# Kernel optimization log

Measured on AMD Instinct MI355X. Metric: run time of the kernel, lower is better.

The kernel has to match this reference:

```python
import jax, jax.numpy as jnp
import numpy as np

D_MODEL = 512
NUM_HEADS = 8
DEPTH = D_MODEL // NUM_HEADS


def setup_inputs() -> dict:
    key = jax.random.key(0)
    ks = jax.random.split(key, 11)
    B, S = 2, 4096
    scale = 1.0 / np.sqrt(D_MODEL)
    inp = {
        "q": jax.random.normal(ks[0], (B, S, D_MODEL), jnp.float32),
        "k": jax.random.normal(ks[1], (B, S, D_MODEL), jnp.float32),
        "v": jax.random.normal(ks[2], (B, S, D_MODEL), jnp.float32),
        "wq_w": jax.random.normal(ks[3], (D_MODEL, D_MODEL), jnp.float32) * scale,
        "wq_b": jnp.zeros((D_MODEL,), jnp.float32),
        "wk_w": jax.random.normal(ks[4], (D_MODEL, D_MODEL), jnp.float32) * scale,
        "wk_b": jnp.zeros((D_MODEL,), jnp.float32),
        "wv_w": jax.random.normal(ks[5], (D_MODEL, D_MODEL), jnp.float32) * scale,
        "wv_b": jnp.zeros((D_MODEL,), jnp.float32),
        "wo_w": jax.random.normal(ks[6], (D_MODEL, D_MODEL), jnp.float32) * scale,
        "wo_b": jnp.zeros((D_MODEL,), jnp.float32),
    }
    return inp


def _split_heads(x):
    # [B, S, D] -> [B, H, S, depth]
    B, S, _ = x.shape
    return x.reshape(B, S, NUM_HEADS, DEPTH).transpose(0, 2, 1, 3)


def reference(q, k, v, wq_w, wq_b, wk_w, wk_b, wv_w, wv_b, wo_w, wo_b):
    B, S, _ = q.shape
    qh = _split_heads(q @ wq_w.T + wq_b)  # [B,H,S,d]
    kh = _split_heads(k @ wk_w.T + wk_b)
    vh = _split_heads(v @ wv_w.T + wv_b)
    logits = jnp.einsum('bhqd,bhkd->bhqk', qh, kh) / jnp.sqrt(
        jnp.asarray(DEPTH, jnp.float32))
    attn = jax.nn.softmax(logits, axis=-1)
    out = jnp.einsum('bhqk,bhkd->bhqd', attn, vh)  # [B,H,S,d]
    out = out.transpose(0, 2, 1, 3).reshape(B, S, D_MODEL)
    return out @ wo_w.T + wo_b
```

## Files before the change

kernel.cpp:

```cpp
#include <hip/hip_runtime.h>

typedef __attribute__((ext_vector_type(8))) short short8;
typedef __attribute__((ext_vector_type(4))) float float4v;

#define D_MODEL 512
#define NUM_HEADS 8
#define DEPTH 64
#define SEQ 4096
#define BATCH 2
#define MROWS 8192
#define SCALE_Q 0.18033688011112043f

#define SW(r, c) (((r) * 64) + ((((c) ^ ((r) & 7))) * 8))
#define SW128(n, c) (((n) * 128) + ((((c) ^ ((n) & 15))) * 8))

static __device__ __forceinline__ unsigned short f2bf(float f) {
  unsigned int u = __builtin_bit_cast(unsigned int, f);
  u += 0x7FFFu + ((u >> 16) & 1u);
  return (unsigned short)(u >> 16);
}
static __device__ __forceinline__ unsigned int pk2(float a, float b) {
  return (unsigned int)f2bf(a) | ((unsigned int)f2bf(b) << 16);
}
static __device__ __forceinline__ unsigned int pk2f(float a, float b) {
  unsigned int ua = __builtin_bit_cast(unsigned int, a) + 0x8000u;
  unsigned int ub = __builtin_bit_cast(unsigned int, b) + 0x8000u;
  return __builtin_amdgcn_perm(ub, ua, 0x07060302u);
}

struct CvtArgs {
  const float4v* src[7];
  uint2* dst[7];
  int n4[7];
};
__global__ __launch_bounds__(256) void cvt_all(CvtArgs a) {
  const int ti = blockIdx.y;
  const float4v* __restrict__ s = a.src[ti];
  uint2* __restrict__ d = a.dst[ti];
  const int n = a.n4[ti];
  for (int i = blockIdx.x * 256 + threadIdx.x; i < n; i += gridDim.x * 256) {
    float4v f = s[i];
    d[i] = make_uint2(pk2(f[0], f[1]), pk2(f[2], f[3]));
  }
}

struct QkvArgs {
  const unsigned short* X[3];
  const unsigned short* W[3];
  const float* bias[3];
  unsigned short* out[3];
};
__global__ __launch_bounds__(256) void gemm128_qkv(QkvArgs a) {
  __shared__ unsigned short smem[2 * 128 * 64];
  unsigned short* As = smem;
  unsigned short* Bs = smem + 128 * 64;
  const int z = blockIdx.z;
  const unsigned short* __restrict__ X = a.X[z];
  const unsigned short* __restrict__ W = a.W[z];
  const float* __restrict__ bias = a.bias[z];
  unsigned short* __restrict__ out = a.out[z];
  const int t = threadIdx.x;
  const int w = t >> 6, l = t & 63, lq = l >> 4, lm = l & 15;
  const int mq = (w & 1) * 64, nq = (w >> 1) * 64;
  const int mBase = blockIdx.x * 128, nBase = blockIdx.y * 128;
  float4v acc[4][4] = {};
  for (int kc = 0; kc < D_MODEL; kc += 64) {
    __syncthreads();
#pragma unroll
    for (int p = 0; p < 4; ++p) {
      int i = p * 256 + t, r = i >> 3, c = i & 7;
      *(short8*)&As[SW(r, c)] = *(const short8*)&X[(size_t)(mBase + r) * D_MODEL + kc + c * 8];
      *(short8*)&Bs[SW(r, c)] = *(const short8*)&W[(size_t)(nBase + r) * D_MODEL + kc + c * 8];
    }
    __syncthreads();
#pragma unroll
    for (int kk = 0; kk < 2; ++kk) {
      short8 av[4];
#pragma unroll
      for (int fm = 0; fm < 4; ++fm)
        av[fm] = *(const short8*)&As[SW(mq + fm * 16 + lm, kk * 4 + lq)];
#pragma unroll
      for (int fn = 0; fn < 4; ++fn) {
        short8 bv = *(const short8*)&Bs[SW(nq + fn * 16 + lm, kk * 4 + lq)];
#pragma unroll
        for (int fm = 0; fm < 4; ++fm)
          acc[fm][fn] = __builtin_amdgcn_mfma_f32_16x16x32_bf16(av[fm], bv, acc[fm][fn], 0, 0, 0);
      }
    }
  }
  if (z == 2) {
    __syncthreads();
    unsigned short* T = smem;
#pragma unroll
    for (int fn = 0; fn < 4; ++fn) {
      int n = nq + fn * 16 + lm;
      float bv = bias[nBase + n];
#pragma unroll
      for (int fm = 0; fm < 4; ++fm) {
        int m0 = mq + fm * 16 + lq * 4;
        uint2 u;
        u.x = pk2(acc[fm][fn][0] + bv, acc[fm][fn][1] + bv);
        u.y = pk2(acc[fm][fn][2] + bv, acc[fm][fn][3] + bv);
        *(uint2*)&T[SW128(n, m0 >> 3) + (lq & 1) * 4] = u;
      }
    }
    __syncthreads();
    const int bb = mBase >> 12, s0 = mBase & 4095;
#pragma unroll
    for (int p = 0; p < 8; ++p) {
      int i = p * 256 + t, n = i >> 4, cm = i & 15;
      int gn = nBase + n, h = gn >> 6, d = gn & 63;
      *(short8*)&out[(((size_t)(bb * NUM_HEADS + h) * DEPTH + d) << 12) + s0 + cm * 8] =
          *(const short8*)&T[SW128(n, cm)];
    }
  } else {
    const float scale = (z == 0) ? SCALE_Q : 1.0f;
#pragma unroll
    for (int fn = 0; fn < 4; ++fn) {
      int gn = nBase + nq + fn * 16 + lm;
      float bv = bias[gn];
      int h = gn >> 6, d = gn & 63;
#pragma unroll
      for (int fm = 0; fm < 4; ++fm) {
#pragma unroll
        for (int r = 0; r < 4; ++r) {
          int gm = mBase + mq + fm * 16 + lq * 4 + r;
          int bb = gm >> 12, s = gm & 4095;
          out[(((size_t)(bb * NUM_HEADS + h) * SEQ + s) << 6) + d] =
              f2bf((acc[fm][fn][r] + bv) * scale);
        }
      }
    }
  }
}

__global__ __launch_bounds__(256) void gemm128_out(
    const unsigned short* __restrict__ X, const unsigned short* __restrict__ W,
    const float* __restrict__ bias, float* __restrict__ out) {
  __shared__ unsigned short smem[2 * 128 * 64];
  unsigned short* As = smem;
  unsigned short* Bs = smem + 128 * 64;
  const int t = threadIdx.x;
  const int w = t >> 6, l = t & 63, lq = l >> 4, lm = l & 15;
  const int mq = (w & 1) * 64, nq = (w >> 1) * 64;
  const int mBase = blockIdx.x * 128, nBase = blockIdx.y * 128;
  float4v acc[4][4] = {};
  for (int kc = 0; kc < D_MODEL; kc += 64) {
    __syncthreads();
#pragma unroll
    for (int p = 0; p < 4; ++p) {
      int i = p * 256 + t, r = i >> 3, c = i & 7;
      *(short8*)&As[SW(r, c)] = *(const short8*)&X[(size_t)(mBase + r) * D_MODEL + kc + c * 8];
      *(short8*)&Bs[SW(r, c)] = *(const short8*)&W[(size_t)(nBase + r) * D_MODEL + kc + c * 8];
    }
    __syncthreads();
#pragma unroll
    for (int kk = 0; kk < 2; ++kk) {
      short8 av[4];
#pragma unroll
      for (int fm = 0; fm < 4; ++fm)
        av[fm] = *(const short8*)&As[SW(mq + fm * 16 + lm, kk * 4 + lq)];
#pragma unroll
      for (int fn = 0; fn < 4; ++fn) {
        short8 bv = *(const short8*)&Bs[SW(nq + fn * 16 + lm, kk * 4 + lq)];
#pragma unroll
        for (int fm = 0; fm < 4; ++fm)
          acc[fm][fn] = __builtin_amdgcn_mfma_f32_16x16x32_bf16(av[fm], bv, acc[fm][fn], 0, 0, 0);
      }
    }
  }
#pragma unroll
  for (int fn = 0; fn < 4; ++fn) {
    int gn = nBase + nq + fn * 16 + lm;
    float bv = bias[gn];
#pragma unroll
    for (int fm = 0; fm < 4; ++fm) {
#pragma unroll
      for (int r = 0; r < 4; ++r) {
        int gm = mBase + mq + fm * 16 + lq * 4 + r;
        out[(size_t)gm * D_MODEL + gn] = acc[fm][fn][r] + bv;
      }
    }
  }
}

struct QkvArgsF {
  const void* X[3];
  const void* W[3];
  const float* bias[3];
  unsigned short* out[3];
};
template <int XFP32, int WFP32>
__global__ __launch_bounds__(256) void gemm_qkv(QkvArgsF a) {
  __shared__ unsigned short As[64 * 72];
  __shared__ unsigned short Bs[64 * 72];
  const int z = blockIdx.z;
  const void* __restrict__ Xv = a.X[z];
  const void* __restrict__ Wv = a.W[z];
  const float* __restrict__ bias = a.bias[z];
  unsigned short* __restrict__ outv = a.out[z];
  const int t = threadIdx.x;
  const int w = t >> 6, l = t & 63, lq = l >> 4, lm = l & 15;
  const int mBase = blockIdx.x * 64;
  const int nBase = blockIdx.y * 64;
  float4v acc[4] = {};
  for (int kc = 0; kc < D_MODEL; kc += 64) {
    __syncthreads();
#pragma unroll
    for (int p = 0; p < 2; ++p) {
      int idx = p * 256 + t;
      int r = idx >> 3, c = (idx & 7) * 8;
      if (XFP32) {
        const float* Xf = (const float*)Xv;
        float4v f0 = *(const float4v*)&Xf[(size_t)(mBase + r) * D_MODEL + kc + c];
        float4v f1 = *(const float4v*)&Xf[(size_t)(mBase + r) * D_MODEL + kc + c + 4];
        short8 s;
#pragma unroll
        for (int j = 0; j < 4; ++j) { s[j] = (short)f2bf(f0[j]); s[4 + j] = (short)f2bf(f1[j]); }
        *(short8*)&As[r * 72 + c] = s;
      } else {
        *(short8*)&As[r * 72 + c] =
            *(const short8*)&((const unsigned short*)Xv)[(size_t)(mBase + r) * D_MODEL + kc + c];
      }
      if (WFP32) {
        const float* Wf = (const float*)Wv;
        float4v f0 = *(const float4v*)&Wf[(size_t)(nBase + r) * D_MODEL + kc + c];
        float4v f1 = *(const float4v*)&Wf[(size_t)(nBase + r) * D_MODEL + kc + c + 4];
        short8 s;
#pragma unroll
        for (int j = 0; j < 4; ++j) { s[j] = (short)f2bf(f0[j]); s[4 + j] = (short)f2bf(f1[j]); }
        *(short8*)&Bs[r * 72 + c] = s;
      } else {
        *(short8*)&Bs[r * 72 + c] =
            *(const short8*)&((const unsigned short*)Wv)[(size_t)(nBase + r) * D_MODEL + kc + c];
      }
    }
    __syncthreads();
#pragma unroll
    for (int kk = 0; kk < 64; kk += 32) {
      short8 av = *(const short8*)&As[(w * 16 + lm) * 72 + kk + lq * 8];
#pragma unroll
      for (int f = 0; f < 4; ++f) {
        short8 b = *(const short8*)&Bs[(f * 16 + lm) * 72 + kk + lq * 8];
        acc[f] = __builtin_amdgcn_mfma_f32_16x16x32_bf16(av, b, acc[f], 0, 0, 0);
      }
    }
  }
  if (z == 2) {
    __syncthreads();
    unsigned short* T = As;
#pragma unroll
    for (int f = 0; f < 4; ++f) {
      int dl = f * 16 + lm;
      float bv = bias[nBase + dl];
      uint2 u;
      u.x = pk2(acc[f][0] + bv, acc[f][1] + bv);
      u.y = pk2(acc[f][2] + bv, acc[f][3] + bv);
      int chunk = 2 * w + (lq >> 1);
      *(uint2*)&T[SW(dl, chunk) + (lq & 1) * 4] = u;
    }
    __syncthreads();
    const int bb = mBase >> 12, s0v = mBase & 4095, h = nBase >> 6;
    const size_t vbase = ((size_t)(bb * NUM_HEADS + h)) * DEPTH * SEQ;
#pragma unroll
    for (int p = 0; p < 2; ++p) {
      int idx = p * 256 + t;
      int d = idx >> 3, c = idx & 7;
      *(short8*)&outv[vbase + (size_t)d * SEQ + s0v + c * 8] = *(const short8*)&T[SW(d, c)];
    }
  } else {
    const float scale = (z == 0) ? SCALE_Q : 1.0f;
#pragma unroll
    for (int f = 0; f < 4; ++f) {
      int gn = nBase + f * 16 + lm;
      float bv = bias[gn];
#pragma unroll
      for (int r = 0; r < 4; ++r) {
        int gm = mBase + w * 16 + lq * 4 + r;
        float v = (acc[f][r] + bv) * scale;
        int bb = gm >> 12, s = gm & 4095;
        int h = gn >> 6, d = gn & 63;
        outv[(((size_t)(bb * NUM_HEADS + h) * SEQ + s) << 6) + d] = f2bf(v);
      }
    }
  }
}

__global__ __launch_bounds__(256) void gemm_out_f(
    const unsigned short* __restrict__ Xb, const float* __restrict__ Wf,
    const float* __restrict__ bias, float* __restrict__ out) {
  __shared__ unsigned short As[64 * 72];
  __shared__ unsigned short Bs[64 * 72];
  const int t = threadIdx.x;
  const int w = t >> 6, l = t & 63, lq = l >> 4, lm = l & 15;
  const int mBase = blockIdx.x * 64;
  const int nBase = blockIdx.y * 64;
  float4v acc[4] = {};
  for (int kc = 0; kc < D_MODEL; kc += 64) {
    __syncthreads();
#pragma unroll
    for (int p = 0; p < 2; ++p) {
      int idx = p * 256 + t;
      int r = idx >> 3, c = (idx & 7) * 8;
      *(short8*)&As[r * 72 + c] =
          *(const short8*)&Xb[(size_t)(mBase + r) * D_MODEL + kc + c];
      float4v f0 = *(const float4v*)&Wf[(size_t)(nBase + r) * D_MODEL + kc + c];
      float4v f1 = *(const float4v*)&Wf[(size_t)(nBase + r) * D_MODEL + kc + c + 4];
      short8 s;
#pragma unroll
      for (int j = 0; j < 4; ++j) { s[j] = (short)f2bf(f0[j]); s[4 + j] = (short)f2bf(f1[j]); }
      *(short8*)&Bs[r * 72 + c] = s;
    }
    __syncthreads();
#pragma unroll
    for (int kk = 0; kk < 64; kk += 32) {
      short8 av = *(const short8*)&As[(w * 16 + lm) * 72 + kk + lq * 8];
#pragma unroll
      for (int f = 0; f < 4; ++f) {
        short8 b = *(const short8*)&Bs[(f * 16 + lm) * 72 + kk + lq * 8];
        acc[f] = __builtin_amdgcn_mfma_f32_16x16x32_bf16(av, b, acc[f], 0, 0, 0);
      }
    }
  }
#pragma unroll
  for (int f = 0; f < 4; ++f) {
    int gn = nBase + f * 16 + lm;
    float bv = bias[gn];
#pragma unroll
    for (int r = 0; r < 4; ++r) {
      int gm = mBase + w * 16 + lq * 4 + r;
      out[(size_t)gm * D_MODEL + gn] = acc[f][r] + bv;
    }
  }
}

__global__ __launch_bounds__(256) void attn(
    const unsigned short* __restrict__ Qh,
    const unsigned short* __restrict__ Kh,
    const unsigned short* __restrict__ Vt,
    unsigned short* __restrict__ AO)
{
  __shared__ unsigned short Ksub[2][64 * 64];
  __shared__ unsigned short Vsub[2][64 * 64];
  __shared__ unsigned short Psub[128 * 64];
  const int t = threadIdx.x;
  const int w = t >> 6;
  const int l = t & 63, lq = l >> 4, lm = l & 15;
  const int bh = blockIdx.y;
  const size_t base = (size_t)bh * SEQ * DEPTH;
  const int qbase = blockIdx.x * 128 + w * 32;
  const unsigned short* __restrict__ Kp = Kh + base;
  const unsigned short* __restrict__ Vp = Vt + base;

  short8 qf[2][2];
#pragma unroll
  for (int qb = 0; qb < 2; ++qb)
#pragma unroll
    for (int kk = 0; kk < 2; ++kk)
      qf[qb][kk] = *(const short8*)&Qh[base + (size_t)(qbase + qb * 16 + lm) * DEPTH + kk * 32 + lq * 8];

  short8 ones;
#pragma unroll
  for (int j = 0; j < 8; ++j) ones[j] = (short)0x3F80;

  float4v oacc[2][4] = {};
  float4v sumacc[2] = {};
  short8 kreg[2], vreg[2];

#pragma unroll
  for (int p = 0; p < 2; ++p) {
    int i = p * 256 + t, r = i >> 3, c = i & 7;
    kreg[p] = *(const short8*)&Kp[(size_t)r * DEPTH + c * 8];
    vreg[p] = *(const short8*)&Vp[(size_t)r * SEQ + c * 8];
  }
#pragma unroll
  for (int p = 0; p < 2; ++p) {
    int i = p * 256 + t, r = i >> 3, c = i & 7;
    *(short8*)&Ksub[0][SW(r, c)] = kreg[p];
    *(short8*)&Vsub[0][SW(r, c)] = vreg[p];
  }
  __syncthreads();

  for (int it = 0; it < 64; ++it) {
    const int cur = it & 1;
    if (it < 63) {
      const int s0n = (it + 1) * 64;
#pragma unroll
      for (int p = 0; p < 2; ++p) {
        int i = p * 256 + t, r = i >> 3, c = i & 7;
        kreg[p] = *(const short8*)&Kp[(size_t)(s0n + r) * DEPTH + c * 8];
        vreg[p] = *(const short8*)&Vp[(size_t)r * SEQ + s0n + c * 8];
      }
    }
#pragma unroll
    for (int f = 0; f < 4; ++f) {
      float4v sacc[2] = {};
#pragma unroll
      for (int kk = 0; kk < 2; ++kk) {
        short8 a = *(const short8*)&Ksub[cur][SW(f * 16 + lm, kk * 4 + lq)];
        sacc[0] = __builtin_amdgcn_mfma_f32_16x16x32_bf16(a, qf[0][kk], sacc[0], 0, 0, 0);
        sacc[1] = __builtin_amdgcn_mfma_f32_16x16x32_bf16(a, qf[1][kk], sacc[1], 0, 0, 0);
      }
#pragma unroll
      for (int qb = 0; qb < 2; ++qb) {
        uint2 u;
        u.x = pk2f(__builtin_amdgcn_exp2f(sacc[qb][0]), __builtin_amdgcn_exp2f(sacc[qb][1]));
        u.y = pk2f(__builtin_amdgcn_exp2f(sacc[qb][2]), __builtin_amdgcn_exp2f(sacc[qb][3]));
        *(uint2*)&Psub[SW(w * 32 + qb * 16 + lm, 2 * f + (lq >> 1)) + (lq & 1) * 4] = u;
      }
    }
#pragma unroll
    for (int kk = 0; kk < 2; ++kk) {
      short8 a0 = *(const short8*)&Psub[SW(w * 32 + lm, kk * 4 + lq)];
      short8 a1 = *(const short8*)&Psub[SW(w * 32 + 16 + lm, kk * 4 + lq)];
      sumacc[0] = __builtin_amdgcn_mfma_f32_16x16x32_bf16(a0, ones, sumacc[0], 0, 0, 0);
      sumacc[1] = __builtin_amdgcn_mfma_f32_16x16x32_bf16(a1, ones, sumacc[1], 0, 0, 0);
#pragma unroll
      for (int df = 0; df < 4; ++df) {
        short8 b = *(const short8*)&Vsub[cur][SW(df * 16 + lm, kk * 4 + lq)];
        oacc[0][df] = __builtin_amdgcn_mfma_f32_16x16x32_bf16(a0, b, oacc[0][df], 0, 0, 0);
        oacc[1][df] = __builtin_amdgcn_mfma_f32_16x16x32_bf16(a1, b, oacc[1][df], 0, 0, 0);
      }
    }
    if (it < 63) {
#pragma unroll
      for (int p = 0; p < 2; ++p) {
        int i = p * 256 + t, r = i >> 3, c = i & 7;
        *(short8*)&Ksub[cur ^ 1][SW(r, c)] = kreg[p];
        *(short8*)&Vsub[cur ^ 1][SW(r, c)] = vreg[p];
      }
    }
    __syncthreads();
  }
  const int bb = bh >> 3, h = bh & 7;
#pragma unroll
  for (int qb = 0; qb < 2; ++qb) {
#pragma unroll
    for (int r = 0; r < 4; ++r) {
      float rinv = 1.0f / sumacc[qb][r];
      int s = qbase + qb * 16 + lq * 4 + r;
#pragma unroll
      for (int df = 0; df < 4; ++df) {
        int d = df * 16 + lm;
        AO[((size_t)(bb * SEQ + s)) * D_MODEL + h * DEPTH + d] = f2bf(oacc[qb][df][r] * rinv);
      }
    }
  }
}

extern "C" void kernel_launch(void* const* d_in, const int* in_sizes, int n_in,
                              void* d_out, int out_size, void* d_ws, size_t ws_size,
                              hipStream_t stream) {
  const void* q = d_in[0];
  const void* k = d_in[1];
  const void* v = d_in[2];
  const float* wq = (const float*)d_in[3];
  const float* bq = (const float*)d_in[4];
  const float* wk = (const float*)d_in[5];
  const float* bk = (const float*)d_in[6];
  const float* wv = (const float*)d_in[7];
  const float* bv = (const float*)d_in[8];
  const float* wo = (const float*)d_in[9];
  const float* bo = (const float*)d_in[10];

  const size_t HSD = (size_t)BATCH * NUM_HEADS * SEQ * DEPTH;
  const size_t WSZ = (size_t)D_MODEL * D_MODEL;
  unsigned short* ws = (unsigned short*)d_ws;
  unsigned short* Qh = ws;
  unsigned short* Kh = Qh + HSD;
  unsigned short* Vt = Kh + HSD;
  unsigned short* AO = Vt + HSD;
  unsigned short* Wc[4] = {AO + HSD, AO + HSD + WSZ, AO + HSD + 2 * WSZ, AO + HSD + 3 * WSZ};
  unsigned short* Xc[3] = {Wc[3] + WSZ, Wc[3] + WSZ + HSD, Wc[3] + WSZ + 2 * HSD};
  const int tier = (ws_size >= (7 * HSD + 4 * WSZ) * 2) ? 1
                 : (ws_size >= (4 * HSD + 4 * WSZ) * 2) ? 2 : 3;

  const float* wptr[4] = {wq, wk, wv, wo};
  const void* xin[3] = {q, k, v};

  if (tier < 3) {
    CvtArgs ca = {};
    int ny = 0;
    if (tier == 1) {
      for (int i = 0; i < 3; ++i) {
        ca.src[ny] = (const float4v*)xin[i];
        ca.dst[ny] = (uint2*)Xc[i];
        ca.n4[ny++] = (int)(HSD / 4);
      }
    }
    for (int i = 0; i < 4; ++i) {
      ca.src[ny] = (const float4v*)wptr[i];
      ca.dst[ny] = (uint2*)Wc[i];
      ca.n4[ny++] = (int)(WSZ / 4);
    }
    cvt_all<<<dim3(512, ny), 256, 0, stream>>>(ca);
  }

  if (tier == 1) {
    QkvArgs qa;
    for (int i = 0; i < 3; ++i) { qa.X[i] = Xc[i]; qa.W[i] = Wc[i]; }
    qa.bias[0] = bq; qa.bias[1] = bk; qa.bias[2] = bv;
    qa.out[0] = Qh; qa.out[1] = Kh; qa.out[2] = Vt;
    gemm128_qkv<<<dim3(MROWS / 128, D_MODEL / 128, 3), 256, 0, stream>>>(qa);
  } else {
    QkvArgsF qa;
    for (int i = 0; i < 3; ++i) qa.X[i] = xin[i];
    qa.bias[0] = bq; qa.bias[1] = bk; qa.bias[2] = bv;
    qa.out[0] = Qh; qa.out[1] = Kh; qa.out[2] = Vt;
    dim3 g(MROWS / 64, D_MODEL / 64, 3);
    if (tier == 2) {
      for (int i = 0; i < 3; ++i) qa.W[i] = Wc[i];
      gemm_qkv<1, 0><<<g, 256, 0, stream>>>(qa);
    } else {
      for (int i = 0; i < 3; ++i) qa.W[i] = wptr[i];
      gemm_qkv<1, 1><<<g, 256, 0, stream>>>(qa);
    }
  }

  attn<<<dim3(SEQ / 128, BATCH * NUM_HEADS), 256, 0, stream>>>(Qh, Kh, Vt, AO);

  if (tier < 3)
    gemm128_out<<<dim3(MROWS / 128, D_MODEL / 128), 256, 0, stream>>>(AO, Wc[3], bo, (float*)d_out);
  else
    gemm_out_f<<<dim3(MROWS / 64, D_MODEL / 64), 256, 0, stream>>>(AO, wo, bo, (float*)d_out);
}
```

Measured before the change: 243.8 us.

## Fuse fp32-to-bf16 conversion into GEMM loads and drop separate convert pass

Removes the standalone cvt_all kernel and the tiered workspace paths. The 128x128 QKV GEMM and a new 128x64 output GEMM now read fp32 inputs and weights directly and convert them to bf16 while filling shared memory. This avoids writing and re-reading bf16 copies of the activations and saves one launch, at the cost of reading twice as many bytes per tile load plus conversion ALU work inside the GEMMs. The attention loop is also manually unrolled by two so the double-buffer index is a compile-time constant.

```diff
diff --git a/kernel.cpp b/kernel.cpp
--- a/kernel.cpp
+++ b/kernel.cpp
@@ -27,36 +27,31 @@
   unsigned int ub = __builtin_bit_cast(unsigned int, b) + 0x8000u;
   return __builtin_amdgcn_perm(ub, ua, 0x07060302u);
 }
-
-struct CvtArgs {
-  const float4v* src[7];
-  uint2* dst[7];
-  int n4[7];
-};
-__global__ __launch_bounds__(256) void cvt_all(CvtArgs a) {
-  const int ti = blockIdx.y;
-  const float4v* __restrict__ s = a.src[ti];
-  uint2* __restrict__ d = a.dst[ti];
-  const int n = a.n4[ti];
-  for (int i = blockIdx.x * 256 + threadIdx.x; i < n; i += gridDim.x * 256) {
-    float4v f = s[i];
-    d[i] = make_uint2(pk2(f[0], f[1]), pk2(f[2], f[3]));
-  }
-}
-
-struct QkvArgs {
-  const unsigned short* X[3];
-  const unsigned short* W[3];
+static __device__ __forceinline__ short8 cvt8(const float* p) {
+  float4v f0 = *(const float4v*)p;
+  float4v f1 = *(const float4v*)(p + 4);
+  short8 s;
+#pragma unroll
+  for (int j = 0; j < 4; ++j) {
+    s[j] = (short)f2bf(f0[j]);
+    s[4 + j] = (short)f2bf(f1[j]);
+  }
+  return s;
+}
+
+struct QkvA {
+  const float* X[3];
+  const float* W[3];
   const float* bias[3];
   unsigned short* out[3];
 };
-__global__ __launch_bounds__(256) void gemm128_qkv(QkvArgs a) {
+__global__ __launch_bounds__(256) void gemm128_qkv(QkvA a) {
   __shared__ unsigned short smem[2 * 128 * 64];
   unsigned short* As = smem;
   unsigned short* Bs = smem + 128 * 64;
   const int z = blockIdx.z;
-  const unsigned short* __restrict__ X = a.X[z];
-  const unsigned short* __restrict__ W = a.W[z];
+  const float* __restrict__ X = a.X[z];
+  const float* __restrict__ W = a.W[z];
   const float* __restrict__ bias = a.bias[z];
   unsigned short* __restrict__ out = a.out[z];
   const int t = threadIdx.x;
@@ -69,8 +64,8 @@
 #pragma unroll
     for (int p = 0; p < 4; ++p) {
       int i = p * 256 + t, r = i >> 3, c = i & 7;
-      *(short8*)&As[SW(r, c)] = *(const short8*)&X[(size_t)(mBase + r) * D_MODEL + kc + c * 8];
-      *(short8*)&Bs[SW(r, c)] = *(const short8*)&W[(size_t)(nBase + r) * D_MODEL + kc + c * 8];
+      *(short8*)&As[SW(r, c)] = cvt8(&X[(size_t)(mBase + r) * D_MODEL + kc + c * 8]);
+      *(short8*)&Bs[SW(r, c)] = cvt8(&W[(size_t)(nBase + r) * D_MODEL + kc + c * 8]);
     }
     __syncthreads();
 #pragma unroll
@@ -134,202 +129,57 @@
   }
 }
 
-__global__ __launch_bounds__(256) void gemm128_out(
-    const unsigned short* __restrict__ X, const unsigned short* __restrict__ W,
-    const float* __restrict__ bias, float* __restrict__ out) {
-  __shared__ unsigned short smem[2 * 128 * 64];
-  unsigned short* As = smem;
-  unsigned short* Bs = smem + 128 * 64;
+__global__ __launch_bounds__(256) void gemm_out_128x64(
+    const unsigned short* __restrict__ X,
+    const float* __restrict__ W,
+    const float* __restrict__ bias,
+    float* __restrict__ out) {
+  __shared__ unsigned short As[128 * 64];
+  __shared__ unsigned short Bs[64 * 64];
   const int t = threadIdx.x;
   const int w = t >> 6, l = t & 63, lq = l >> 4, lm = l & 15;
-  const int mq = (w & 1) * 64, nq = (w >> 1) * 64;
-  const int mBase = blockIdx.x * 128, nBase = blockIdx.y * 128;
-  float4v acc[4][4] = {};
+  const int mq = w * 32;
+  const int mBase = blockIdx.x * 128, nBase = blockIdx.y * 64;
+  float4v acc[2][4] = {};
   for (int kc = 0; kc < D_MODEL; kc += 64) {
     __syncthreads();
 #pragma unroll
     for (int p = 0; p < 4; ++p) {
       int i = p * 256 + t, r = i >> 3, c = i & 7;
       *(short8*)&As[SW(r, c)] = *(const short8*)&X[(size_t)(mBase + r) * D_MODEL + kc + c * 8];
-      *(short8*)&Bs[SW(r, c)] = *(const short8*)&W[(size_t)(nBase + r) * D_MODEL + kc + c * 8];
+    }
+#pragma unroll
+    for (int p = 0; p < 2; ++p) {
+      int i = p * 256 + t, r = i >> 3, c = i & 7;
+      *(short8*)&Bs[SW(r, c)] = cvt8(&W[(size_t)(nBase + r) * D_MODEL + kc + c * 8]);
     }
     __syncthreads();
 #pragma unroll
     for (int kk = 0; kk < 2; ++kk) {
-      short8 av[4];
-#pragma unroll
-      for (int fm = 0; fm < 4; ++fm)
+      short8 av[2];
+#pragma unroll
+      for (int fm = 0; fm < 2; ++fm)
         av[fm] = *(const short8*)&As[SW(mq + fm * 16 + lm, kk * 4 + lq)];
 #pragma unroll
       for (int fn = 0; fn < 4; ++fn) {
-        short8 bv = *(const short8*)&Bs[SW(nq + fn * 16 + lm, kk * 4 + lq)];
-#pragma unroll
-        for (int fm = 0; fm < 4; ++fm)
+        short8 bv = *(const short8*)&Bs[SW(fn * 16 + lm, kk * 4 + lq)];
+#pragma unroll
+        for (int fm = 0; fm < 2; ++fm)
           acc[fm][fn] = __builtin_amdgcn_mfma_f32_16x16x32_bf16(av[fm], bv, acc[fm][fn], 0, 0, 0);
       }
     }
   }
 #pragma unroll
   for (int fn = 0; fn < 4; ++fn) {
-    int gn = nBase + nq + fn * 16 + lm;
+    int gn = nBase + fn * 16 + lm;
     float bv = bias[gn];
 #pragma unroll
-    for (int fm = 0; fm < 4; ++fm) {
+    for (int fm = 0; fm < 2; ++fm) {
 #pragma unroll
       for (int r = 0; r < 4; ++r) {
         int gm = mBase + mq + fm * 16 + lq * 4 + r;
         out[(size_t)gm * D_MODEL + gn] = acc[fm][fn][r] + bv;
       }
-    }
-  }
-}
-
-struct QkvArgsF {
-  const void* X[3];
-  const void* W[3];
-  const float* bias[3];
-  unsigned short* out[3];
-};
-template <int XFP32, int WFP32>
-__global__ __launch_bounds__(256) void gemm_qkv(QkvArgsF a) {
-  __shared__ unsigned short As[64 * 72];
-  __shared__ unsigned short Bs[64 * 72];
-  const int z = blockIdx.z;
-  const void* __restrict__ Xv = a.X[z];
-  const void* __restrict__ Wv = a.W[z];
-  const float* __restrict__ bias = a.bias[z];
-  unsigned short* __restrict__ outv = a.out[z];
-  const int t = threadIdx.x;
-  const int w = t >> 6, l = t & 63, lq = l >> 4, lm = l & 15;
-  const int mBase = blockIdx.x * 64;
-  const int nBase = blockIdx.y * 64;
-  float4v acc[4] = {};
-  for (int kc = 0; kc < D_MODEL; kc += 64) {
-    __syncthreads();
-#pragma unroll
-    for (int p = 0; p < 2; ++p) {
-      int idx = p * 256 + t;
-      int r = idx >> 3, c = (idx & 7) * 8;
-      if (XFP32) {
-        const float* Xf = (const float*)Xv;
-        float4v f0 = *(const float4v*)&Xf[(size_t)(mBase + r) * D_MODEL + kc + c];
-        float4v f1 = *(const float4v*)&Xf[(size_t)(mBase + r) * D_MODEL + kc + c + 4];
-        short8 s;
-#pragma unroll
-        for (int j = 0; j < 4; ++j) { s[j] = (short)f2bf(f0[j]); s[4 + j] = (short)f2bf(f1[j]); }
-        *(short8*)&As[r * 72 + c] = s;
-      } else {
-        *(short8*)&As[r * 72 + c] =
-            *(const short8*)&((const unsigned short*)Xv)[(size_t)(mBase + r) * D_MODEL + kc + c];
-      }
-      if (WFP32) {
-        const float* Wf = (const float*)Wv;
-        float4v f0 = *(const float4v*)&Wf[(size_t)(nBase + r) * D_MODEL + kc + c];
-        float4v f1 = *(const float4v*)&Wf[(size_t)(nBase + r) * D_MODEL + kc + c + 4];
-        short8 s;
-#pragma unroll
-        for (int j = 0; j < 4; ++j) { s[j] = (short)f2bf(f0[j]); s[4 + j] = (short)f2bf(f1[j]); }
-        *(short8*)&Bs[r * 72 + c] = s;
-      } else {
-        *(short8*)&Bs[r * 72 + c] =
-            *(const short8*)&((const unsigned short*)Wv)[(size_t)(nBase + r) * D_MODEL + kc + c];
-      }
-    }
-    __syncthreads();
-#pragma unroll
-    for (int kk = 0; kk < 64; kk += 32) {
-      short8 av = *(const short8*)&As[(w * 16 + lm) * 72 + kk + lq * 8];
-#pragma unroll
-      for (int f = 0; f < 4; ++f) {
-        short8 b = *(const short8*)&Bs[(f * 16 + lm) * 72 + kk + lq * 8];
-        acc[f] = __builtin_amdgcn_mfma_f32_16x16x32_bf16(av, b, acc[f], 0, 0, 0);
-      }
-    }
-  }
-  if (z == 2) {
-    __syncthreads();
-    unsigned short* T = As;
-#pragma unroll
-    for (int f = 0; f < 4; ++f) {
-      int dl = f * 16 + lm;
-      float bv = bias[nBase + dl];
-      uint2 u;
-      u.x = pk2(acc[f][0] + bv, acc[f][1] + bv);
-      u.y = pk2(acc[f][2] + bv, acc[f][3] + bv);
-      int chunk = 2 * w + (lq >> 1);
-      *(uint2*)&T[SW(dl, chunk) + (lq & 1) * 4] = u;
-    }
-    __syncthreads();
-    const int bb = mBase >> 12, s0v = mBase & 4095, h = nBase >> 6;
-    const size_t vbase = ((size_t)(bb * NUM_HEADS + h)) * DEPTH * SEQ;
-#pragma unroll
-    for (int p = 0; p < 2; ++p) {
-      int idx = p * 256 + t;
-      int d = idx >> 3, c = idx & 7;
-      *(short8*)&outv[vbase + (size_t)d * SEQ + s0v + c * 8] = *(const short8*)&T[SW(d, c)];
-    }
-  } else {
-    const float scale = (z == 0) ? SCALE_Q : 1.0f;
-#pragma unroll
-    for (int f = 0; f < 4; ++f) {
-      int gn = nBase + f * 16 + lm;
-      float bv = bias[gn];
-#pragma unroll
-      for (int r = 0; r < 4; ++r) {
-        int gm = mBase + w * 16 + lq * 4 + r;
-        float v = (acc[f][r] + bv) * scale;
-        int bb = gm >> 12, s = gm & 4095;
-        int h = gn >> 6, d = gn & 63;
-        outv[(((size_t)(bb * NUM_HEADS + h) * SEQ + s) << 6) + d] = f2bf(v);
-      }
-    }
-  }
-}
-
-__global__ __launch_bounds__(256) void gemm_out_f(
-    const unsigned short* __restrict__ Xb, const float* __restrict__ Wf,
-    const float* __restrict__ bias, float* __restrict__ out) {
-  __shared__ unsigned short As[64 * 72];
-  __shared__ unsigned short Bs[64 * 72];
-  const int t = threadIdx.x;
-  const int w = t >> 6, l = t & 63, lq = l >> 4, lm = l & 15;
-  const int mBase = blockIdx.x * 64;
-  const int nBase = blockIdx.y * 64;
-  float4v acc[4] = {};
-  for (int kc = 0; kc < D_MODEL; kc += 64) {
-    __syncthreads();
-#pragma unroll
-    for (int p = 0; p < 2; ++p) {
-      int idx = p * 256 + t;
-      int r = idx >> 3, c = (idx & 7) * 8;
-      *(short8*)&As[r * 72 + c] =
-          *(const short8*)&Xb[(size_t)(mBase + r) * D_MODEL + kc + c];
-      float4v f0 = *(const float4v*)&Wf[(size_t)(nBase + r) * D_MODEL + kc + c];
-      float4v f1 = *(const float4v*)&Wf[(size_t)(nBase + r) * D_MODEL + kc + c + 4];
-      short8 s;
-#pragma unroll
-      for (int j = 0; j < 4; ++j) { s[j] = (short)f2bf(f0[j]); s[4 + j] = (short)f2bf(f1[j]); }
-      *(short8*)&Bs[r * 72 + c] = s;
-    }
-    __syncthreads();
-#pragma unroll
-    for (int kk = 0; kk < 64; kk += 32) {
-      short8 av = *(const short8*)&As[(w * 16 + lm) * 72 + kk + lq * 8];
-#pragma unroll
-      for (int f = 0; f < 4; ++f) {
-        short8 b = *(const short8*)&Bs[(f * 16 + lm) * 72 + kk + lq * 8];
-        acc[f] = __builtin_amdgcn_mfma_f32_16x16x32_bf16(av, b, acc[f], 0, 0, 0);
-      }
-    }
-  }
-#pragma unroll
-  for (int f = 0; f < 4; ++f) {
-    int gn = nBase + f * 16 + lm;
-    float bv = bias[gn];
-#pragma unroll
-    for (int r = 0; r < 4; ++r) {
-      int gm = mBase + w * 16 + lq * 4 + r;
-      out[(size_t)gm * D_MODEL + gn] = acc[f][r] + bv;
     }
   }
 }
@@ -381,10 +231,9 @@
   }
   __syncthreads();
 
-  for (int it = 0; it < 64; ++it) {
-    const int cur = it & 1;
-    if (it < 63) {
-      const int s0n = (it + 1) * 64;
+  auto step = [&](int cur, int tile, bool pf) {
+    if (pf) {
+      const int s0n = (tile + 1) * 64;
 #pragma unroll
       for (int p = 0; p < 2; ++p) {
         int i = p * 256 + t, r = i >> 3, c = i & 7;
@@ -422,7 +271,7 @@
         oacc[1][df] = __builtin_amdgcn_mfma_f32_16x16x32_bf16(a1, b, oacc[1][df], 0, 0, 0);
       }
     }
-    if (it < 63) {
+    if (pf) {
 #pragma unroll
       for (int p = 0; p < 2; ++p) {
         int i = p * 256 + t, r = i >> 3, c = i & 7;
@@ -431,7 +280,13 @@
       }
     }
     __syncthreads();
-  }
+  };
+
+  for (int it = 0; it < 64; it += 2) {
+    step(0, it, true);
+    step(1, it + 1, it + 2 < 64);
+  }
+
   const int bb = bh >> 3, h = bh & 7;
 #pragma unroll
   for (int qb = 0; qb < 2; ++qb) {
@@ -451,9 +306,9 @@
 extern "C" void kernel_launch(void* const* d_in, const int* in_sizes, int n_in,
                               void* d_out, int out_size, void* d_ws, size_t ws_size,
                               hipStream_t stream) {
-  const void* q = d_in[0];
-  const void* k = d_in[1];
-  const void* v = d_in[2];
+  const float* q = (const float*)d_in[0];
+  const float* k = (const float*)d_in[1];
+  const float* v = (const float*)d_in[2];
   const float* wq = (const float*)d_in[3];
   const float* bq = (const float*)d_in[4];
   const float* wk = (const float*)d_in[5];
@@ -464,63 +319,20 @@
   const float* bo = (const float*)d_in[10];
 
   const size_t HSD = (size_t)BATCH * NUM_HEADS * SEQ * DEPTH;
-  const size_t WSZ = (size_t)D_MODEL * D_MODEL;
   unsigned short* ws = (unsigned short*)d_ws;
   unsigned short* Qh = ws;
   unsigned short* Kh = Qh + HSD;
   unsigned short* Vt = Kh + HSD;
   unsigned short* AO = Vt + HSD;
-  unsigned short* Wc[4] = {AO + HSD, AO + HSD + WSZ, AO + HSD + 2 * WSZ, AO + HSD + 3 * WSZ};
-  unsigned short* Xc[3] = {Wc[3] + WSZ, Wc[3] + WSZ + HSD, Wc[3] + WSZ + 2 * HSD};
-  const int tier = (ws_size >= (7 * HSD + 4 * WSZ) * 2) ? 1
-                 : (ws_size >= (4 * HSD + 4 * WSZ) * 2) ? 2 : 3;
-
-  const float* wptr[4] = {wq, wk, wv, wo};
-  const void* xin[3] = {q, k, v};
-
-  if (tier < 3) {
-    CvtArgs ca = {};
-    int ny = 0;
-    if (tier == 1) {
-      for (int i = 0; i < 3; ++i) {
-        ca.src[ny] = (const float4v*)xin[i];
-        ca.dst[ny] = (uint2*)Xc[i];
-        ca.n4[ny++] = (int)(HSD / 4);
-      }
-    }
-    for (int i = 0; i < 4; ++i) {
-      ca.src[ny] = (const float4v*)wptr[i];
-      ca.dst[ny] = (uint2*)Wc[i];
-      ca.n4[ny++] = (int)(WSZ / 4);
-    }
-    cvt_all<<<dim3(512, ny), 256, 0, stream>>>(ca);
-  }
-
-  if (tier == 1) {
-    QkvArgs qa;
-    for (int i = 0; i < 3; ++i) { qa.X[i] = Xc[i]; qa.W[i] = Wc[i]; }
-    qa.bias[0] = bq; qa.bias[1] = bk; qa.bias[2] = bv;
-    qa.out[0] = Qh; qa.out[1] = Kh; qa.out[2] = Vt;
-    gemm128_qkv<<<dim3(MROWS / 128, D_MODEL / 128, 3), 256, 0, stream>>>(qa);
-  } else {
-    QkvArgsF qa;
-    for (int i = 0; i < 3; ++i) qa.X[i] = xin[i];
-    qa.bias[0] = bq; qa.bias[1] = bk; qa.bias[2] = bv;
-    qa.out[0] = Qh; qa.out[1] = Kh; qa.out[2] = Vt;
-    dim3 g(MROWS / 64, D_MODEL / 64, 3);
-    if (tier == 2) {
-      for (int i = 0; i < 3; ++i) qa.W[i] = Wc[i];
-      gemm_qkv<1, 0><<<g, 256, 0, stream>>>(qa);
-    } else {
-      for (int i = 0; i < 3; ++i) qa.W[i] = wptr[i];
-      gemm_qkv<1, 1><<<g, 256, 0, stream>>>(qa);
-    }
-  }
+
+  QkvA qa;
+  qa.X[0] = q; qa.X[1] = k; qa.X[2] = v;
+  qa.W[0] = wq; qa.W[1] = wk; qa.W[2] = wv;
+  qa.bias[0] = bq; qa.bias[1] = bk; qa.bias[2] = bv;
+  qa.out[0] = Qh; qa.out[1] = Kh; qa.out[2] = Vt;
+  gemm128_qkv<<<dim3(MROWS / 128, D_MODEL / 128, 3), 256, 0, stream>>>(qa);
 
   attn<<<dim3(SEQ / 128, BATCH * NUM_HEADS), 256, 0, stream>>>(Qh, Kh, Vt, AO);
 
-  if (tier < 3)
-    gemm128_out<<<dim3(MROWS / 128, D_MODEL / 128), 256, 0, stream>>>(AO, Wc[3], bo, (float*)d_out);
-  else
-    gemm_out_f<<<dim3(MROWS / 64, D_MODEL / 64), 256, 0, stream>>>(AO, wo, bo, (float*)d_out);
-}
+  gemm_out_128x64<<<dim3(MROWS / 128, D_MODEL / 64), 256, 0, stream>>>(AO, wo, bo, (float*)d_out);
+}
```

Measured after the change: 274.7 us. 12.6% more time.
